# Performance work log

Measured on AMD Instinct MI355X. Metric: run time of the kernel, lower is better.

Reference implementation:

```python
import jax, jax.numpy as jnp
import numpy as np

DELTA = 10.0
EPS = 1e-08
THRESHOLD = 0.9
STEEPNESS = 10.0


def setup_inputs() -> dict:
    key = jax.random.key(0)
    k1, k2 = jax.random.split(key)
    B, T2, T1, F = 16, 2048, 512, 128
    mels = jax.random.normal(k1, (B, T2, F), dtype=jnp.float32)
    alpha = jax.random.uniform(k2, (B, T2, T1), dtype=jnp.float32)
    mel_mask = jnp.ones((B, T2), dtype=jnp.int32)
    text_mask = jnp.ones((B, T1), dtype=jnp.int32)
    return {"mels": mels, "alpha": alpha, "mel_mask": mel_mask, "text_mask": text_mask}


def reference(mels, alpha, mel_mask, text_mask):
    B, T2, F = mels.shape
    T1 = text_mask.shape[-1]
    audio_mask = mel_mask.astype(bool)
    txt_mask = text_mask.astype(bool)
    am_f = audio_mask.astype(alpha.dtype)  # [B, T2]
    tm_f = txt_mask.astype(alpha.dtype)    # [B, T1]

    # index vector p: [B, T1]
    p = jnp.broadcast_to(jnp.arange(T1, dtype=alpha.dtype), (B, T1))

    # cosine similarity between consecutive frames (F.normalize: x / max(||x||, 1e-12))
    norm = jnp.maximum(jnp.linalg.norm(mels, axis=-1, keepdims=True), 1e-12)
    z_norm = mels / norm
    cosine_sim = jnp.sum(z_norm[:, :-1] * z_norm[:, 1:], axis=-1)  # [B, T2-1]
    activity = jax.nn.sigmoid(STEEPNESS * (THRESHOLD - cosine_sim))
    activity = jnp.concatenate([jnp.ones((B, 1), dtype=activity.dtype), activity], axis=-1)
    activity = activity * am_f

    # soft monotonic index via gated cumsum of alpha-proposal increments
    imv_proposal = jnp.einsum('bts,bs->bt', alpha, p)  # [B, T2]
    delta_prop = jnp.concatenate(
        [jnp.zeros((B, 1), dtype=imv_proposal.dtype), jnp.diff(imv_proposal, axis=-1)], axis=-1)
    eff_delta = jnp.clip(delta_prop * activity, 0.0, 1.0)
    imv = jnp.cumsum(eff_delta, axis=-1) * am_f

    # rescale so last valid frame maps to last phoneme index
    last_idx = jnp.maximum(audio_mask.sum(-1).astype(jnp.int32) - 1, 0)  # [B]
    last_val = jnp.maximum(jnp.take_along_axis(imv, last_idx[:, None], axis=1)[:, 0], 1e-06)
    text_len = txt_mask.sum(-1).astype(imv.dtype)
    scale = jnp.maximum(text_len - 1.0, 0.0) / last_val
    imv = imv * scale[:, None] * am_f

    # gamma: masked softmax over phonemes of -delta * (imv - p)^2
    dist_sq = (imv[:, :, None] - p[:, None, :]) ** 2  # [B, T2, T1]
    logits = jnp.where(txt_mask[:, None, :], -DELTA * dist_sq, -1e9)
    gamma = jax.nn.softmax(logits, axis=-1) * am_f[:, :, None]

    # durations: soft mass per phoneme
    durations = jnp.sum(gamma * am_f[:, :, None], axis=1) * tm_f  # [B, T1]

    # attention-pooling of mel frames onto phonemes
    w = jnp.swapaxes(gamma, 1, 2) * am_f[:, None, :]  # [B, T1, T2]
    w = w / (jnp.sum(w, axis=-1, keepdims=True) + EPS)
    aligned_mels = jnp.einsum('bst,btf->bsf', w, mels) * tm_f[:, :, None]  # [B, T1, F]
    return aligned_mels, durations, imv
```

## Files before the change

### kernel.cpp

```cpp
#include <hip/hip_runtime.h>
#include <math.h>
#include <cstddef>

#define B_  16
#define T2_ 2048
#define T1_ 512
#define F_  128

constexpr float DELTA_C = 10.0f;
constexpr float EPS_C   = 1e-8f;
constexpr float THRESH_C = 0.9f;
constexpr float STEEP_C  = 10.0f;

__device__ __forceinline__ float wave_reduce_sum(float v) {
    for (int off = 32; off > 0; off >>= 1) v += __shfl_xor(v, off, 64);
    return v;
}

__global__ __launch_bounds__(256) void act_kernel(const float* __restrict__ mels,
                                                  const int* __restrict__ mel_mask,
                                                  float* __restrict__ act) {
    int wid  = (int)((blockIdx.x * blockDim.x + threadIdx.x) >> 6);
    int lane = threadIdx.x & 63;
    if (wid >= B_ * T2_) return;
    int t = wid % T2_;
    float a_val;
    if (t == 0) {
        a_val = 1.0f;
    } else {
        const float2* r0 = (const float2*)(mels + (size_t)(wid - 1) * F_);
        const float2* r1 = (const float2*)(mels + (size_t)wid * F_);
        float2 x = r0[lane];
        float2 y = r1[lane];
        float d  = x.x * y.x + x.y * y.y;
        float n0 = x.x * x.x + x.y * x.y;
        float n1 = y.x * y.x + y.y * y.y;
        for (int off = 32; off > 0; off >>= 1) {
            d  += __shfl_xor(d, off, 64);
            n0 += __shfl_xor(n0, off, 64);
            n1 += __shfl_xor(n1, off, 64);
        }
        float cs = d / (fmaxf(sqrtf(n0), 1e-12f) * fmaxf(sqrtf(n1), 1e-12f));
        a_val = 1.0f / (1.0f + __expf(-STEEP_C * (THRESH_C - cs)));
    }
    if (lane == 0) act[wid] = a_val * (float)mel_mask[wid];
}

__global__ __launch_bounds__(256) void prop_kernel(const float* __restrict__ alpha,
                                                   float* __restrict__ prop) {
    int wid  = (int)((blockIdx.x * blockDim.x + threadIdx.x) >> 6);
    int lane = threadIdx.x & 63;
    if (wid >= B_ * T2_) return;
    const float4* row = (const float4*)(alpha + (size_t)wid * T1_);
    float4 v0 = row[lane * 2];
    float4 v1 = row[lane * 2 + 1];
    float s0 = (float)(lane * 8);
    float sum = v0.x * s0 + v0.y * (s0 + 1.0f) + v0.z * (s0 + 2.0f) + v0.w * (s0 + 3.0f)
              + v1.x * (s0 + 4.0f) + v1.y * (s0 + 5.0f) + v1.z * (s0 + 6.0f) + v1.w * (s0 + 7.0f);
    sum = wave_reduce_sum(sum);
    if (lane == 0) prop[wid] = sum;
}

__global__ __launch_bounds__(256) void scan_kernel(const float* __restrict__ prop,
                                                   const float* __restrict__ act,
                                                   const int* __restrict__ mel_mask,
                                                   const int* __restrict__ text_mask,
                                                   float* __restrict__ imv_out,
                                                   float* __restrict__ Zout) {
    int b   = blockIdx.x;
    int tid = threadIdx.x;
    __shared__ float s_imv[T2_];
    __shared__ float s_part[256];
    __shared__ int s_am, s_tm;
    if (tid == 0) { s_am = 0; s_tm = 0; }
    __syncthreads();

    const float* pr = prop + (size_t)b * T2_;
    const float* ac = act + (size_t)b * T2_;
    const int*   mm = mel_mask + (size_t)b * T2_;
    const int*   tm = text_mask + (size_t)b * T1_;

    float e[8];
    int t0 = tid * 8;
    int am_local = 0;
    float run = 0.0f;
    for (int i = 0; i < 8; i++) {
        int t = t0 + i;
        float d = (t == 0) ? 0.0f : (pr[t] - pr[t - 1]) * ac[t];
        d = fminf(fmaxf(d, 0.0f), 1.0f);
        run += d;
        e[i] = run;
        am_local += mm[t];
    }
    s_part[tid] = run;
    atomicAdd(&s_am, am_local);
    atomicAdd(&s_tm, tm[tid] + tm[tid + 256]);
    __syncthreads();

    for (int off = 1; off < 256; off <<= 1) {
        float u = (tid >= off) ? s_part[tid - off] : 0.0f;
        __syncthreads();
        s_part[tid] += u;
        __syncthreads();
    }
    float excl = (tid == 0) ? 0.0f : s_part[tid - 1];
    for (int i = 0; i < 8; i++) {
        int t = t0 + i;
        s_imv[t] = (e[i] + excl) * (float)mm[t];
    }
    __syncthreads();

    int last_idx = max(s_am - 1, 0);
    float last_val = fmaxf(s_imv[last_idx], 1e-6f);
    float scale = fmaxf((float)s_tm - 1.0f, 0.0f) / last_val;

    for (int i = 0; i < 8; i++) {
        int t = t0 + i;
        float v = s_imv[t] * scale * (float)mm[t];
        imv_out[(size_t)b * T2_ + t] = v;
        int c = (int)floorf(v);
        float Z = 0.0f;
        for (int s = c - 2; s <= c + 3; s++) {
            if (s >= 0 && s < T1_ && tm[s]) {
                float dd = v - (float)s;
                Z += __expf(-DELTA_C * dd * dd);
            }
        }
        Zout[(size_t)b * T2_ + t] = fmaxf(Z, 1e-30f);
    }
}

__global__ __launch_bounds__(256) void pool_kernel(const float* __restrict__ mels,
                                                   const int* __restrict__ mel_mask,
                                                   const int* __restrict__ text_mask,
                                                   const float* __restrict__ imv,
                                                   const float* __restrict__ Z,
                                                   float* __restrict__ aligned,
                                                   float* __restrict__ dur) {
    int wid  = (int)((blockIdx.x * blockDim.x + threadIdx.x) >> 6);
    int lane = threadIdx.x & 63;
    if (wid >= B_ * T1_) return;
    int b = wid / T1_, s = wid % T1_;
    const float* iv = imv + (size_t)b * T2_;

    float lo_v = (float)s - 3.0f, hi_v = (float)s + 3.0f;
    int lo = 0, hi = T2_;
    while (lo < hi) { int mid = (lo + hi) >> 1; if (iv[mid] >= lo_v) hi = mid; else lo = mid + 1; }
    int t_lo = lo;
    lo = t_lo; hi = T2_;
    while (lo < hi) { int mid = (lo + hi) >> 1; if (iv[mid] > hi_v) hi = mid; else lo = mid + 1; }
    int t_hi = lo;

    const float* zz = Z + (size_t)b * T2_;
    const int*   mm = mel_mask + (size_t)b * T2_;
    float2 acc = {0.0f, 0.0f};
    float gsum = 0.0f;
    for (int t = t_lo; t < t_hi; t++) {
        float d = iv[t] - (float)s;
        float g = (float)mm[t] * __expf(-DELTA_C * d * d) / zz[t];
        gsum += g;
        float2 m = ((const float2*)(mels + ((size_t)b * T2_ + t) * F_))[lane];
        acc.x += g * m.x;
        acc.y += g * m.y;
    }
    float tmv = (float)text_mask[(size_t)b * T1_ + s];
    float inv = tmv / (gsum + EPS_C);
    float2 outv = {acc.x * inv, acc.y * inv};
    ((float2*)(aligned + ((size_t)b * T1_ + s) * F_))[lane] = outv;
    if (lane == 0) dur[(size_t)b * T1_ + s] = gsum * tmv;
}

extern "C" void kernel_launch(void* const* d_in, const int* in_sizes, int n_in,
                              void* d_out, int out_size, void* d_ws, size_t ws_size,
                              hipStream_t stream) {
    const float* mels      = (const float*)d_in[0];
    const float* alpha     = (const float*)d_in[1];
    const int*   mel_mask  = (const int*)d_in[2];
    const int*   text_mask = (const int*)d_in[3];

    float* out     = (float*)d_out;
    float* aligned = out;
    float* dur     = out + (size_t)B_ * T1_ * F_;
    float* imv     = dur + (size_t)B_ * T1_;

    float* ws   = (float*)d_ws;
    float* act  = ws;
    float* prop = ws + (size_t)B_ * T2_;
    float* Z    = ws + 2 * (size_t)B_ * T2_;

    dim3 blk(256);
    act_kernel <<<(B_ * T2_) / 4, blk, 0, stream>>>(mels, mel_mask, act);
    prop_kernel<<<(B_ * T2_) / 4, blk, 0, stream>>>(alpha, prop);
    scan_kernel<<<B_, blk, 0, stream>>>(prop, act, mel_mask, text_mask, imv, Z);
    pool_kernel<<<(B_ * T1_) / 4, blk, 0, stream>>>(mels, mel_mask, text_mask, imv, Z, aligned, dur);
}
```

Before: 146.9 us.

## Fuse activity and proposal kernels, pack imv with inverse Z, unroll pooling

Merges the cosine-activity and alpha-proposal kernels into one launch that does a single shuffle reduction over four values, and switches the alpha loads to a lane-contiguous float4 pattern. The scan kernel replaces shared-memory atomics with wave shuffles, and writes a packed (imv, 1/Z) pair in which masked frames get a sentinel imv and zero weight. The pooling kernel reads that packed array instead of separate imv, Z and mask arrays, and unrolls the frame loop by four so loads can overlap. The sentinel changes the binary-search semantics for masked frames and needs workspace room for the float2 array.

```diff
diff --git a/kernel.cpp b/kernel.cpp
--- a/kernel.cpp
+++ b/kernel.cpp
@@ -7,58 +7,56 @@
 #define T1_ 512
 #define F_  128
 
-constexpr float DELTA_C = 10.0f;
-constexpr float EPS_C   = 1e-8f;
+constexpr float DELTA_C  = 10.0f;
+constexpr float EPS_C    = 1e-8f;
 constexpr float THRESH_C = 0.9f;
 constexpr float STEEP_C  = 10.0f;
 
-__device__ __forceinline__ float wave_reduce_sum(float v) {
-    for (int off = 32; off > 0; off >>= 1) v += __shfl_xor(v, off, 64);
-    return v;
-}
-
-__global__ __launch_bounds__(256) void act_kernel(const float* __restrict__ mels,
-                                                  const int* __restrict__ mel_mask,
-                                                  float* __restrict__ act) {
+__global__ __launch_bounds__(256) void actprop_kernel(const float* __restrict__ mels,
+                                                      const float* __restrict__ alpha,
+                                                      const int* __restrict__ mel_mask,
+                                                      float* __restrict__ act,
+                                                      float* __restrict__ prop) {
     int wid  = (int)((blockIdx.x * blockDim.x + threadIdx.x) >> 6);
     int lane = threadIdx.x & 63;
     if (wid >= B_ * T2_) return;
     int t = wid % T2_;
-    float a_val;
-    if (t == 0) {
-        a_val = 1.0f;
-    } else {
-        const float2* r0 = (const float2*)(mels + (size_t)(wid - 1) * F_);
-        const float2* r1 = (const float2*)(mels + (size_t)wid * F_);
-        float2 x = r0[lane];
-        float2 y = r1[lane];
-        float d  = x.x * y.x + x.y * y.y;
-        float n0 = x.x * x.x + x.y * x.y;
-        float n1 = y.x * y.x + y.y * y.y;
-        for (int off = 32; off > 0; off >>= 1) {
-            d  += __shfl_xor(d, off, 64);
-            n0 += __shfl_xor(n0, off, 64);
-            n1 += __shfl_xor(n1, off, 64);
+
+    const float4* row = (const float4*)(alpha + (size_t)wid * T1_);
+    float4 v0 = row[lane];
+    float4 v1 = row[lane + 64];
+
+    float d = 0.f, n0 = 0.f, n1 = 0.f;
+    if (t > 0) {
+        float2 x = ((const float2*)(mels + (size_t)(wid - 1) * F_))[lane];
+        float2 y = ((const float2*)(mels + (size_t)wid * F_))[lane];
+        d  = x.x * y.x + x.y * y.y;
+        n0 = x.x * x.x + x.y * x.y;
+        n1 = y.x * y.x + y.y * y.y;
+    }
+
+    float fL = (float)(lane * 4);
+    float psum = v0.x * fL + v0.y * (fL + 1.f) + v0.z * (fL + 2.f) + v0.w * (fL + 3.f)
+               + v1.x * (fL + 256.f) + v1.y * (fL + 257.f) + v1.z * (fL + 258.f) + v1.w * (fL + 259.f);
+
+    for (int off = 32; off > 0; off >>= 1) {
+        psum += __shfl_xor(psum, off, 64);
+        d    += __shfl_xor(d,    off, 64);
+        n0   += __shfl_xor(n0,   off, 64);
+        n1   += __shfl_xor(n1,   off, 64);
+    }
+
+    if (lane == 0) {
+        float a_val;
+        if (t == 0) {
+            a_val = 1.0f;
+        } else {
+            float cs = d / (fmaxf(sqrtf(n0), 1e-12f) * fmaxf(sqrtf(n1), 1e-12f));
+            a_val = 1.0f / (1.0f + __expf(-STEEP_C * (THRESH_C - cs)));
         }
-        float cs = d / (fmaxf(sqrtf(n0), 1e-12f) * fmaxf(sqrtf(n1), 1e-12f));
-        a_val = 1.0f / (1.0f + __expf(-STEEP_C * (THRESH_C - cs)));
-    }
-    if (lane == 0) act[wid] = a_val * (float)mel_mask[wid];
-}
-
-__global__ __launch_bounds__(256) void prop_kernel(const float* __restrict__ alpha,
-                                                   float* __restrict__ prop) {
-    int wid  = (int)((blockIdx.x * blockDim.x + threadIdx.x) >> 6);
-    int lane = threadIdx.x & 63;
-    if (wid >= B_ * T2_) return;
-    const float4* row = (const float4*)(alpha + (size_t)wid * T1_);
-    float4 v0 = row[lane * 2];
-    float4 v1 = row[lane * 2 + 1];
-    float s0 = (float)(lane * 8);
-    float sum = v0.x * s0 + v0.y * (s0 + 1.0f) + v0.z * (s0 + 2.0f) + v0.w * (s0 + 3.0f)
-              + v1.x * (s0 + 4.0f) + v1.y * (s0 + 5.0f) + v1.z * (s0 + 6.0f) + v1.w * (s0 + 7.0f);
-    sum = wave_reduce_sum(sum);
-    if (lane == 0) prop[wid] = sum;
+        act[wid]  = a_val * (float)mel_mask[wid];
+        prop[wid] = psum;
+    }
 }
 
 __global__ __launch_bounds__(256) void scan_kernel(const float* __restrict__ prop,
@@ -66,18 +64,17 @@
                                                    const int* __restrict__ mel_mask,
                                                    const int* __restrict__ text_mask,
                                                    float* __restrict__ imv_out,
-                                                   float* __restrict__ Zout) {
-    int b   = blockIdx.x;
-    int tid = threadIdx.x;
+                                                   float2* __restrict__ packed) {
+    int b    = blockIdx.x;
+    int tid  = threadIdx.x;
+    int wave = tid >> 6, lane = tid & 63;
     __shared__ float s_imv[T2_];
     __shared__ float s_part[256];
-    __shared__ int s_am, s_tm;
-    if (tid == 0) { s_am = 0; s_tm = 0; }
-    __syncthreads();
+    __shared__ int   s_am4[4], s_tm4[4];
 
     const float* pr = prop + (size_t)b * T2_;
-    const float* ac = act + (size_t)b * T2_;
-    const int*   mm = mel_mask + (size_t)b * T2_;
+    const float* ac = act  + (size_t)b * T2_;
+    const int*   mm = mel_mask  + (size_t)b * T2_;
     const int*   tm = text_mask + (size_t)b * T1_;
 
     float e[8];
@@ -92,9 +89,13 @@
         e[i] = run;
         am_local += mm[t];
     }
+    int tm_local = tm[tid] + tm[tid + 256];
+    for (int off = 32; off > 0; off >>= 1) {
+        am_local += __shfl_xor(am_local, off, 64);
+        tm_local += __shfl_xor(tm_local, off, 64);
+    }
+    if (lane == 0) { s_am4[wave] = am_local; s_tm4[wave] = tm_local; }
     s_part[tid] = run;
-    atomicAdd(&s_am, am_local);
-    atomicAdd(&s_tm, tm[tid] + tm[tid + 256]);
     __syncthreads();
 
     for (int off = 1; off < 256; off <<= 1) {
@@ -110,13 +111,16 @@
     }
     __syncthreads();
 
-    int last_idx = max(s_am - 1, 0);
+    int am_total = s_am4[0] + s_am4[1] + s_am4[2] + s_am4[3];
+    int tm_total = s_tm4[0] + s_tm4[1] + s_tm4[2] + s_tm4[3];
+    int last_idx = max(am_total - 1, 0);
     float last_val = fmaxf(s_imv[last_idx], 1e-6f);
-    float scale = fmaxf((float)s_tm - 1.0f, 0.0f) / last_val;
+    float scale = fmaxf((float)tm_total - 1.0f, 0.0f) / last_val;
 
     for (int i = 0; i < 8; i++) {
         int t = t0 + i;
-        float v = s_imv[t] * scale * (float)mm[t];
+        int valid = mm[t];
+        float v = s_imv[t] * scale * (float)valid;
         imv_out[(size_t)b * T2_ + t] = v;
         int c = (int)floorf(v);
         float Z = 0.0f;
@@ -126,46 +130,65 @@
                 Z += __expf(-DELTA_C * dd * dd);
             }
         }
-        Zout[(size_t)b * T2_ + t] = fmaxf(Z, 1e-30f);
+        Z = fmaxf(Z, 1e-30f);
+        float2 pk;
+        pk.x = valid ? v : 3.0e4f;
+        pk.y = valid ? (1.0f / Z) : 0.0f;
+        packed[(size_t)b * T2_ + t] = pk;
     }
 }
 
 __global__ __launch_bounds__(256) void pool_kernel(const float* __restrict__ mels,
-                                                   const int* __restrict__ mel_mask,
                                                    const int* __restrict__ text_mask,
-                                                   const float* __restrict__ imv,
-                                                   const float* __restrict__ Z,
+                                                   const float2* __restrict__ packed,
                                                    float* __restrict__ aligned,
                                                    float* __restrict__ dur) {
     int wid  = (int)((blockIdx.x * blockDim.x + threadIdx.x) >> 6);
     int lane = threadIdx.x & 63;
     if (wid >= B_ * T1_) return;
     int b = wid / T1_, s = wid % T1_;
-    const float* iv = imv + (size_t)b * T2_;
-
-    float lo_v = (float)s - 3.0f, hi_v = (float)s + 3.0f;
+    const float2* pk   = packed + (size_t)b * T2_;
+    const float2* mel2 = (const float2*)(mels + (size_t)b * T2_ * F_);
+
+    float fs = (float)s;
+    float lo_v = fs - 3.0f, hi_v = fs + 3.0f;
     int lo = 0, hi = T2_;
-    while (lo < hi) { int mid = (lo + hi) >> 1; if (iv[mid] >= lo_v) hi = mid; else lo = mid + 1; }
+    while (lo < hi) { int mid = (lo + hi) >> 1; if (pk[mid].x >= lo_v) hi = mid; else lo = mid + 1; }
     int t_lo = lo;
-    lo = t_lo; hi = T2_;
-    while (lo < hi) { int mid = (lo + hi) >> 1; if (iv[mid] > hi_v) hi = mid; else lo = mid + 1; }
+    hi = T2_;
+    while (lo < hi) { int mid = (lo + hi) >> 1; if (pk[mid].x > hi_v) hi = mid; else lo = mid + 1; }
     int t_hi = lo;
 
-    const float* zz = Z + (size_t)b * T2_;
-    const int*   mm = mel_mask + (size_t)b * T2_;
-    float2 acc = {0.0f, 0.0f};
-    float gsum = 0.0f;
-    for (int t = t_lo; t < t_hi; t++) {
-        float d = iv[t] - (float)s;
-        float g = (float)mm[t] * __expf(-DELTA_C * d * d) / zz[t];
+    float ax = 0.0f, ay = 0.0f, gsum = 0.0f;
+    int t = t_lo;
+    for (; t + 4 <= t_hi; t += 4) {
+        float2 p0 = pk[t], p1 = pk[t + 1], p2 = pk[t + 2], p3 = pk[t + 3];
+        float2 m0 = mel2[(size_t)(t    ) * 64 + lane];
+        float2 m1 = mel2[(size_t)(t + 1) * 64 + lane];
+        float2 m2 = mel2[(size_t)(t + 2) * 64 + lane];
+        float2 m3 = mel2[(size_t)(t + 3) * 64 + lane];
+        float d0 = p0.x - fs, d1 = p1.x - fs, d2 = p2.x - fs, d3 = p3.x - fs;
+        float g0 = __expf(-DELTA_C * d0 * d0) * p0.y;
+        float g1 = __expf(-DELTA_C * d1 * d1) * p1.y;
+        float g2 = __expf(-DELTA_C * d2 * d2) * p2.y;
+        float g3 = __expf(-DELTA_C * d3 * d3) * p3.y;
+        gsum += (g0 + g1) + (g2 + g3);
+        ax += g0 * m0.x + g1 * m1.x + g2 * m2.x + g3 * m3.x;
+        ay += g0 * m0.y + g1 * m1.y + g2 * m2.y + g3 * m3.y;
+    }
+    for (; t < t_hi; t++) {
+        float2 p = pk[t];
+        float2 m = mel2[(size_t)t * 64 + lane];
+        float dd = p.x - fs;
+        float g  = __expf(-DELTA_C * dd * dd) * p.y;
         gsum += g;
-        float2 m = ((const float2*)(mels + ((size_t)b * T2_ + t) * F_))[lane];
-        acc.x += g * m.x;
-        acc.y += g * m.y;
-    }
+        ax += g * m.x;
+        ay += g * m.y;
+    }
+
     float tmv = (float)text_mask[(size_t)b * T1_ + s];
     float inv = tmv / (gsum + EPS_C);
-    float2 outv = {acc.x * inv, acc.y * inv};
+    float2 outv = {ax * inv, ay * inv};
     ((float2*)(aligned + ((size_t)b * T1_ + s) * F_))[lane] = outv;
     if (lane == 0) dur[(size_t)b * T1_ + s] = gsum * tmv;
 }
@@ -183,14 +206,13 @@
     float* dur     = out + (size_t)B_ * T1_ * F_;
     float* imv     = dur + (size_t)B_ * T1_;
 
-    float* ws   = (float*)d_ws;
-    float* act  = ws;
-    float* prop = ws + (size_t)B_ * T2_;
-    float* Z    = ws + 2 * (size_t)B_ * T2_;
+    float*  ws     = (float*)d_ws;
+    float*  act    = ws;
+    float*  prop   = ws + (size_t)B_ * T2_;
+    float2* packed = (float2*)(ws + 2 * (size_t)B_ * T2_);
 
     dim3 blk(256);
-    act_kernel <<<(B_ * T2_) / 4, blk, 0, stream>>>(mels, mel_mask, act);
-    prop_kernel<<<(B_ * T2_) / 4, blk, 0, stream>>>(alpha, prop);
-    scan_kernel<<<B_, blk, 0, stream>>>(prop, act, mel_mask, text_mask, imv, Z);
-    pool_kernel<<<(B_ * T1_) / 4, blk, 0, stream>>>(mels, mel_mask, text_mask, imv, Z, aligned, dur);
-}
+    actprop_kernel<<<(B_ * T2_) / 4, blk, 0, stream>>>(mels, alpha, mel_mask, act, prop);
+    scan_kernel   <<<B_,            blk, 0, stream>>>(prop, act, mel_mask, text_mask, imv, packed);
+    pool_kernel   <<<(B_ * T1_) / 4, blk, 0, stream>>>(mels, text_mask, packed, aligned, dur);
+}
```

Result: faster. 134.3 us (-8.6%).
